# Kernel optimization log

Hardware: AMD Instinct MI355X
Metric: run time of the kernel (lower is better)

Reference implementation:

```python
import jax, jax.numpy as jnp
import numpy as np

N_NODES = 100000


def setup_inputs() -> dict:
    key = jax.random.key(0)
    k_x, k_src, k_dst, k_w = jax.random.split(key, 4)
    X = jax.random.normal(k_x, (N_NODES, 128), dtype=jnp.float32)
    src = jax.random.randint(k_src, (3200000,), 0, N_NODES, dtype=jnp.int64)
    dst = jax.random.randint(k_dst, (3200000,), 0, N_NODES, dtype=jnp.int64)
    # Linear(2*in_channels=256 -> out_channels=128); kaiming-ish scale
    W = jax.random.normal(k_w, (256, 128), dtype=jnp.float32) * (1.0 / np.sqrt(256.0))
    b = jnp.zeros((128,), dtype=jnp.float32)
    return {"X": X, "src": src, "dst": dst, "W": W, "b": b}


def reference(X, src, dst, W, b):
    # G.v2v(X, aggr='mean'): scatter-mean of neighbor features over edges
    msg = X[src]                                              # [E, d] gather
    summed = jax.ops.segment_sum(msg, dst, num_segments=N_NODES)  # [N, d]
    deg = jax.ops.segment_sum(jnp.ones_like(dst, dtype=X.dtype), dst,
                              num_segments=N_NODES)           # [N]
    X_nbr = summed / jnp.maximum(deg, 1.0)[:, None]           # mean, safe for deg=0
    # concat self + neighbor mean, linear, relu (dropout is eval-mode no-op)
    H = jnp.concatenate([X, X_nbr], axis=1)                   # [N, 2d]
    out = jax.nn.relu(H @ W + b)                              # [N, out]
    return out
```

## Files before the change

### kernel.cpp

```cpp
#include <hip/hip_runtime.h>
#include <cstddef>
#include <cstdint>


#define NODES_PER_BLOCK 16
#define PART_SHIFT 8
#define PART_SZ 256
#define MAXP 448
#define CHUNK 4096
#define CAPP 8704

typedef __attribute__((ext_vector_type(8))) short bf16x8;
typedef __attribute__((ext_vector_type(4))) float f32x4;

__device__ __forceinline__ int clampi(int v, int hi) {
    v = v < 0 ? 0 : v;
    return v >= hi ? hi - 1 : v;
}

__device__ __forceinline__ unsigned short bf16_rne(float f) {
    unsigned int u = __float_as_uint(f);
    unsigned int r = (u + 0x7FFFu + ((u >> 16) & 1u)) >> 16;
    return (unsigned short)r;
}

__device__ __forceinline__ unsigned pack2(float a, float b) {
    return (unsigned)bf16_rne(a) | ((unsigned)bf16_rne(b) << 16);
}

__device__ __forceinline__ void acc_bf16x8(float* a, uint4 r) {
    a[0] += __uint_as_float(r.x << 16);
    a[1] += __uint_as_float(r.x & 0xFFFF0000u);
    a[2] += __uint_as_float(r.y << 16);
    a[3] += __uint_as_float(r.y & 0xFFFF0000u);
    a[4] += __uint_as_float(r.z << 16);
    a[5] += __uint_as_float(r.z & 0xFFFF0000u);
    a[6] += __uint_as_float(r.w << 16);
    a[7] += __uint_as_float(r.w & 0xFFFF0000u);
}

__device__ __forceinline__ int wave_excl_scan64(int v, int lane) {
    int x = v;
#pragma unroll
    for (int off = 1; off < 64; off <<= 1) {
        int y = __shfl_up(x, off, 64);
        if (lane >= off) x += y;
    }
    return x - v;
}

__global__ void zero_cursors(int* __restrict__ c, int P) {
    int i = blockIdx.x * blockDim.x + threadIdx.x;
    if (i < P) c[i] = 0;
}

__global__ __launch_bounds__(256) void xw_to_bf16(
    const float* __restrict__ X, unsigned short* __restrict__ Xb, int total4,
    const float* __restrict__ W, unsigned short* __restrict__ Wswz)
{
    int i = blockIdx.x * blockDim.x + threadIdx.x;
    if (i < 256 * 128) {
        int k = i >> 7, n = i & 127;
        int kk = k >> 5, q = (k >> 3) & 3, j = k & 7;
        int cg = n >> 4, nn = n & 15;
        int lane = q * 16 + nn;
        Wswz[((size_t)(kk * 8 + cg) * 64 + lane) * 8 + j] =
            bf16_rne(W[(size_t)k * 128 + n]);
    }
    if (i < total4) {
        float4 v = *(const float4*)(X + (size_t)i * 4);
        ushort4 o;
        o.x = bf16_rne(v.x); o.y = bf16_rne(v.y);
        o.z = bf16_rne(v.z); o.w = bf16_rne(v.w);
        *(ushort4*)(Xb + (size_t)i * 4) = o;
    }
}

__global__ __launch_bounds__(256) void part1(
    const int* __restrict__ src, const int* __restrict__ dst,
    int* __restrict__ cursors, unsigned long long* __restrict__ parts,
    int E, int N, int P)
{
    __shared__ unsigned long long sbuf[CHUNK];
    __shared__ int hist[MAXP], base_s[MAXP], hist2[MAXP], gbase[MAXP];
    const int tid = threadIdx.x;
    const int c0  = blockIdx.x * CHUNK;
    int cnt = E - c0; if (cnt > CHUNK) cnt = CHUNK;

    for (int i = tid; i < P; i += 256) { hist[i] = 0; hist2[i] = 0; }
    __syncthreads();

    int s[16], d[16];
#pragma unroll
    for (int k = 0; k < 16; ++k) {
        int i = k * 256 + tid;
        if (i < cnt) {
            int e = c0 + i;
            d[k] = clampi(dst[e], N);
            s[k] = clampi(src[e], N);
            atomicAdd(&hist[d[k] >> PART_SHIFT], 1);
        } else {
            d[k] = -1; s[k] = 0;
        }
    }
    __syncthreads();

    if (tid < 64) {
        int pref[7]; int run = 0;
#pragma unroll
        for (int k2 = 0; k2 < 7; ++k2) {
            int idx = tid * 7 + k2;
            int v = (idx < P) ? hist[idx] : 0;
            pref[k2] = run; run += v;
        }
        int lx = wave_excl_scan64(run, tid);
#pragma unroll
        for (int k2 = 0; k2 < 7; ++k2) {
            int idx = tid * 7 + k2;
            if (idx < P) base_s[idx] = pref[k2] + lx;
        }
    }
    __syncthreads();

    for (int i = tid; i < P; i += 256) {
        int c = hist[i];
        gbase[i] = (c > 0) ? atomicAdd(&cursors[i], c) : 0;
    }
    __syncthreads();

#pragma unroll
    for (int k = 0; k < 16; ++k) {
        if (d[k] >= 0) {
            int p = d[k] >> PART_SHIFT;
            int pos = atomicAdd(&hist2[p], 1) + base_s[p];
            sbuf[pos] = ((unsigned long long)(unsigned)d[k] << 32) |
                        (unsigned)s[k];
        }
    }
    __syncthreads();

    for (int i = tid; i < cnt; i += 256) {
        unsigned long long rec = sbuf[i];
        int p = ((int)(rec >> 32)) >> PART_SHIFT;
        int gidx = gbase[p] + (i - base_s[p]);
        if (gidx < CAPP) parts[(size_t)p * CAPP + gidx] = rec;
    }
}

__global__ void scan_pbase(const int* __restrict__ cursors,
                           int* __restrict__ pbase, int P)
{
    int tid = threadIdx.x;
    int pref[7]; int run = 0;
#pragma unroll
    for (int k = 0; k < 7; ++k) {
        int idx = tid * 7 + k;
        int v = 0;
        if (idx < P) { v = cursors[idx]; if (v > CAPP) v = CAPP; }
        pref[k] = run; run += v;
    }
    int lx = wave_excl_scan64(run, tid);
#pragma unroll
    for (int k = 0; k < 7; ++k) {
        int idx = tid * 7 + k;
        if (idx < P) pbase[idx] = pref[k] + lx;
    }
}

__global__ __launch_bounds__(256) void part2(
    const unsigned long long* __restrict__ parts,
    const int* __restrict__ cursors, const int* __restrict__ pbase,
    int* __restrict__ csr, int* __restrict__ offsets, int* __restrict__ deg,
    int N, int P)
{
    __shared__ int ldeg[PART_SZ], loff[PART_SZ], lcur[PART_SZ];
    const int p   = blockIdx.x;
    const int tid = threadIdx.x;
    int cnt = cursors[p]; if (cnt > CAPP) cnt = CAPP;
    const int nbase = p << PART_SHIFT;
    const unsigned long long* prec = parts + (size_t)p * CAPP;

    ldeg[tid] = 0; lcur[tid] = 0;
    __syncthreads();
    for (int i = tid; i < cnt; i += 256) {
        int dl = ((int)(prec[i] >> 32)) & (PART_SZ - 1);
        atomicAdd(&ldeg[dl], 1);
    }
    __syncthreads();
    if (tid < 64) {
        int pref[4]; int run = 0;
#pragma unroll
        for (int k = 0; k < 4; ++k) { pref[k] = run; run += ldeg[tid * 4 + k]; }
        int lx = wave_excl_scan64(run, tid);
#pragma unroll
        for (int k = 0; k < 4; ++k) loff[tid * 4 + k] = pref[k] + lx;
    }
    __syncthreads();
    const int pb = pbase[p];
    const int n = nbase + tid;
    if (n < N) { offsets[n] = pb + loff[tid]; deg[n] = ldeg[tid]; }
    for (int i = tid; i < cnt; i += 256) {
        unsigned long long rec = prec[i];
        int dl = ((int)(rec >> 32)) & (PART_SZ - 1);
        int pos = atomicAdd(&lcur[dl], 1);
        csr[pb + loff[dl] + pos] = (int)(rec & 0xFFFFFFFFu);
    }
}

__global__ __launch_bounds__(128) void gather_gemm(
    const unsigned short* __restrict__ Xb,
    const int* __restrict__ csr,
    const int* __restrict__ offsets,
    const int* __restrict__ deg,
    const unsigned short* __restrict__ Wswz,
    const float* __restrict__ bias,
    float* __restrict__ out, int N)
{
    __shared__ unsigned short Hb[NODES_PER_BLOCK][256];
    const int tid = threadIdx.x;
    const int n0  = blockIdx.x * NODES_PER_BLOCK;

    {
        const int sub = tid & 15;
        const int grp = tid >> 4;
        const int f0  = sub * 8;
        for (int ii = 0; ii < 2; ++ii) {
            const int i = grp * 2 + ii;
            const int n = n0 + i;
            if (n >= N) continue;
            const int dg = deg[n];
            const int* brow = csr + offsets[n];
            float acc[8] = {0.f, 0.f, 0.f, 0.f, 0.f, 0.f, 0.f, 0.f};
            int t = 0;
            for (; t + 8 <= dg; t += 8) {
                int i0 = brow[t],     i1 = brow[t + 1];
                int i2 = brow[t + 2], i3 = brow[t + 3];
                int i4 = brow[t + 4], i5 = brow[t + 5];
                int i6 = brow[t + 6], i7 = brow[t + 7];
                uint4 r0 = *(const uint4*)(Xb + (size_t)i0 * 128 + f0);
                uint4 r1 = *(const uint4*)(Xb + (size_t)i1 * 128 + f0);
                uint4 r2 = *(const uint4*)(Xb + (size_t)i2 * 128 + f0);
                uint4 r3 = *(const uint4*)(Xb + (size_t)i3 * 128 + f0);
                uint4 r4 = *(const uint4*)(Xb + (size_t)i4 * 128 + f0);
                uint4 r5 = *(const uint4*)(Xb + (size_t)i5 * 128 + f0);
                uint4 r6 = *(const uint4*)(Xb + (size_t)i6 * 128 + f0);
                uint4 r7 = *(const uint4*)(Xb + (size_t)i7 * 128 + f0);
                acc_bf16x8(acc, r0); acc_bf16x8(acc, r1);
                acc_bf16x8(acc, r2); acc_bf16x8(acc, r3);
                acc_bf16x8(acc, r4); acc_bf16x8(acc, r5);
                acc_bf16x8(acc, r6); acc_bf16x8(acc, r7);
            }
            for (; t + 4 <= dg; t += 4) {
                int i0 = brow[t],     i1 = brow[t + 1];
                int i2 = brow[t + 2], i3 = brow[t + 3];
                uint4 r0 = *(const uint4*)(Xb + (size_t)i0 * 128 + f0);
                uint4 r1 = *(const uint4*)(Xb + (size_t)i1 * 128 + f0);
                uint4 r2 = *(const uint4*)(Xb + (size_t)i2 * 128 + f0);
                uint4 r3 = *(const uint4*)(Xb + (size_t)i3 * 128 + f0);
                acc_bf16x8(acc, r0); acc_bf16x8(acc, r1);
                acc_bf16x8(acc, r2); acc_bf16x8(acc, r3);
            }
            for (; t < dg; ++t) {
                uint4 r0 = *(const uint4*)(Xb + (size_t)brow[t] * 128 + f0);
                acc_bf16x8(acc, r0);
            }
            const float inv = 1.0f / fmaxf((float)dg, 1.0f);
            *(uint4*)&Hb[i][f0] = *(const uint4*)(Xb + (size_t)n * 128 + f0);
            uint4 mo;
            mo.x = pack2(acc[0] * inv, acc[1] * inv);
            mo.y = pack2(acc[2] * inv, acc[3] * inv);
            mo.z = pack2(acc[4] * inv, acc[5] * inv);
            mo.w = pack2(acc[6] * inv, acc[7] * inv);
            *(uint4*)&Hb[i][128 + f0] = mo;
        }
    }
    __syncthreads();

    const int lane = tid & 63;
    const int wv   = tid >> 6;
    const int m    = lane & 15;
    const int quad = lane >> 4;
    f32x4 acc0 = {0.f, 0.f, 0.f, 0.f};
    f32x4 acc1 = {0.f, 0.f, 0.f, 0.f};
    f32x4 acc2 = {0.f, 0.f, 0.f, 0.f};
    f32x4 acc3 = {0.f, 0.f, 0.f, 0.f};
#pragma unroll
    for (int kk = 0; kk < 8; ++kk) {
        bf16x8 a = *(const bf16x8*)&Hb[m][kk * 32 + quad * 8];
        const unsigned short* wp =
            Wswz + ((size_t)(kk * 8 + wv * 4) * 64 + lane) * 8;
        bf16x8 b0 = *(const bf16x8*)(wp);
        bf16x8 b1 = *(const bf16x8*)(wp + 64 * 8);
        bf16x8 b2 = *(const bf16x8*)(wp + 2 * 64 * 8);
        bf16x8 b3 = *(const bf16x8*)(wp + 3 * 64 * 8);
        acc0 = __builtin_amdgcn_mfma_f32_16x16x32_bf16(a, b0, acc0, 0, 0, 0);
        acc1 = __builtin_amdgcn_mfma_f32_16x16x32_bf16(a, b1, acc1, 0, 0, 0);
        acc2 = __builtin_amdgcn_mfma_f32_16x16x32_bf16(a, b2, acc2, 0, 0, 0);
        acc3 = __builtin_amdgcn_mfma_f32_16x16x32_bf16(a, b3, acc3, 0, 0, 0);
    }
    f32x4 accs[4] = {acc0, acc1, acc2, acc3};
#pragma unroll
    for (int c = 0; c < 4; ++c) {
        int feat = wv * 64 + c * 16 + m;
        float bv = bias[feat];
#pragma unroll
        for (int r = 0; r < 4; ++r) {
            int node = n0 + quad * 4 + r;
            if (node < N)
                out[(size_t)node * 128 + feat] = fmaxf(accs[c][r] + bv, 0.f);
        }
    }
}

static inline size_t align256(size_t x) { return (x + 255) & ~(size_t)255; }

extern "C" void kernel_launch(void* const* d_in, const int* in_sizes, int n_in,
                              void* d_out, int out_size, void* d_ws, size_t ws_size,
                              hipStream_t stream) {
    const float* X    = (const float*)d_in[0];
    const int*   src  = (const int*)d_in[1];
    const int*   dst  = (const int*)d_in[2];
    const float* W    = (const float*)d_in[3];
    const float* bias = (const float*)d_in[4];
    float* out = (float*)d_out;

    const int N = in_sizes[0] / 128;
    const int E = in_sizes[1];
    const int P = (N + PART_SZ - 1) >> PART_SHIFT;

    char* base = (char*)d_ws;
    size_t o_cursors = 0;
    size_t o_pbase   = o_cursors + align256((size_t)P * 4);
    size_t o_deg     = o_pbase   + align256((size_t)P * 4);
    size_t o_off     = o_deg     + align256((size_t)N * 4);
    size_t o_csr     = o_off     + align256((size_t)N * 4);
    size_t o_parts   = o_csr     + align256((size_t)E * 4);
    size_t o_wswz    = o_parts   + align256((size_t)N * 128 * 2);

    int* cursors = (int*)(base + o_cursors);
    int* pbase   = (int*)(base + o_pbase);
    int* deg     = (int*)(base + o_deg);
    int* offsets = (int*)(base + o_off);
    int* csr     = (int*)(base + o_csr);
    unsigned long long* parts = (unsigned long long*)(base + o_parts);
    unsigned short* Xb   = (unsigned short*)(base + o_parts);
    unsigned short* Wswz = (unsigned short*)(base + o_wswz);

    zero_cursors<<<(P + 255) / 256, 256, 0, stream>>>(cursors, P);

    part1<<<(E + CHUNK - 1) / CHUNK, 256, 0, stream>>>(
        src, dst, cursors, parts, E, N, P);

    scan_pbase<<<1, 64, 0, stream>>>(cursors, pbase, P);

    part2<<<P, 256, 0, stream>>>(parts, cursors, pbase, csr, offsets, deg, N, P);

    const int total4 = (N * 128) / 4;
    xw_to_bf16<<<(total4 + 255) / 256, 256, 0, stream>>>(X, Xb, total4, W, Wswz);

    gather_gemm<<<(N + NODES_PER_BLOCK - 1) / NODES_PER_BLOCK, 128, 0, stream>>>(
        Xb, csr, offsets, deg, Wswz, bias, out, N);
}
```

Before: 316.2 us.

## Fuse bf16 conversion into partition kernel, drop pbase scan and second atomic pass

Merges the X/W bf16 conversion into the first partition kernel as extra blocks when the workspace is big enough, so the conversion runs concurrently with edge binning. It also removes the global scan of partition bases by giving each partition a fixed CAPP-sized slot in the CSR array. The second shared-memory atomic pass in part1 is replaced by reusing the ranks returned by the first histogram atomics. The cost is a larger workspace, plus a fallback path that still uses the old aliasing and an extra launch.

```diff
diff --git a/kernel.cpp b/kernel.cpp
--- a/kernel.cpp
+++ b/kernel.cpp
@@ -54,11 +54,11 @@
     if (i < P) c[i] = 0;
 }
 
-__global__ __launch_bounds__(256) void xw_to_bf16(
+__device__ void do_xw_block(int xb,
     const float* __restrict__ X, unsigned short* __restrict__ Xb, int total4,
     const float* __restrict__ W, unsigned short* __restrict__ Wswz)
 {
-    int i = blockIdx.x * blockDim.x + threadIdx.x;
+    int i = xb * 256 + threadIdx.x;
     if (i < 256 * 128) {
         int k = i >> 7, n = i & 127;
         int kk = k >> 5, q = (k >> 3) & 3, j = k & 7;
@@ -76,21 +76,27 @@
     }
 }
 
-__global__ __launch_bounds__(256) void part1(
+__global__ __launch_bounds__(256) void pre1(
     const int* __restrict__ src, const int* __restrict__ dst,
     int* __restrict__ cursors, unsigned long long* __restrict__ parts,
-    int E, int N, int P)
+    int E, int N, int P, int nPart1,
+    const float* __restrict__ X, unsigned short* __restrict__ Xb, int total4,
+    const float* __restrict__ W, unsigned short* __restrict__ Wswz)
 {
+    if ((int)blockIdx.x >= nPart1) {
+        do_xw_block((int)blockIdx.x - nPart1, X, Xb, total4, W, Wswz);
+        return;
+    }
     __shared__ unsigned long long sbuf[CHUNK];
-    __shared__ int hist[MAXP], base_s[MAXP], hist2[MAXP], gbase[MAXP];
+    __shared__ int hist[MAXP], base_s[MAXP], gbase[MAXP];
     const int tid = threadIdx.x;
     const int c0  = blockIdx.x * CHUNK;
     int cnt = E - c0; if (cnt > CHUNK) cnt = CHUNK;
 
-    for (int i = tid; i < P; i += 256) { hist[i] = 0; hist2[i] = 0; }
-    __syncthreads();
-
-    int s[16], d[16];
+    for (int i = tid; i < P; i += 256) hist[i] = 0;
+    __syncthreads();
+
+    int s[16], d[16], r[16];
 #pragma unroll
     for (int k = 0; k < 16; ++k) {
         int i = k * 256 + tid;
@@ -98,9 +104,9 @@
             int e = c0 + i;
             d[k] = clampi(dst[e], N);
             s[k] = clampi(src[e], N);
-            atomicAdd(&hist[d[k] >> PART_SHIFT], 1);
+            r[k] = atomicAdd(&hist[d[k] >> PART_SHIFT], 1);
         } else {
-            d[k] = -1; s[k] = 0;
+            d[k] = -1; s[k] = 0; r[k] = 0;
         }
     }
     __syncthreads();
@@ -132,9 +138,8 @@
     for (int k = 0; k < 16; ++k) {
         if (d[k] >= 0) {
             int p = d[k] >> PART_SHIFT;
-            int pos = atomicAdd(&hist2[p], 1) + base_s[p];
-            sbuf[pos] = ((unsigned long long)(unsigned)d[k] << 32) |
-                        (unsigned)s[k];
+            sbuf[base_s[p] + r[k]] =
+                ((unsigned long long)(unsigned)d[k] << 32) | (unsigned)s[k];
         }
     }
     __syncthreads();
@@ -147,29 +152,9 @@
     }
 }
 
-__global__ void scan_pbase(const int* __restrict__ cursors,
-                           int* __restrict__ pbase, int P)
-{
-    int tid = threadIdx.x;
-    int pref[7]; int run = 0;
-#pragma unroll
-    for (int k = 0; k < 7; ++k) {
-        int idx = tid * 7 + k;
-        int v = 0;
-        if (idx < P) { v = cursors[idx]; if (v > CAPP) v = CAPP; }
-        pref[k] = run; run += v;
-    }
-    int lx = wave_excl_scan64(run, tid);
-#pragma unroll
-    for (int k = 0; k < 7; ++k) {
-        int idx = tid * 7 + k;
-        if (idx < P) pbase[idx] = pref[k] + lx;
-    }
-}
-
 __global__ __launch_bounds__(256) void part2(
     const unsigned long long* __restrict__ parts,
-    const int* __restrict__ cursors, const int* __restrict__ pbase,
+    const int* __restrict__ cursors,
     int* __restrict__ csr, int* __restrict__ offsets, int* __restrict__ deg,
     int N, int P)
 {
@@ -196,7 +181,7 @@
         for (int k = 0; k < 4; ++k) loff[tid * 4 + k] = pref[k] + lx;
     }
     __syncthreads();
-    const int pb = pbase[p];
+    const int pb = p * CAPP;
     const int n = nbase + tid;
     if (n < N) { offsets[n] = pb + loff[tid]; deg[n] = ldeg[tid]; }
     for (int i = tid; i < cnt; i += 256) {
@@ -330,33 +315,42 @@
 
     char* base = (char*)d_ws;
     size_t o_cursors = 0;
-    size_t o_pbase   = o_cursors + align256((size_t)P * 4);
-    size_t o_deg     = o_pbase   + align256((size_t)P * 4);
+    size_t o_deg     = o_cursors + align256((size_t)P * 4);
     size_t o_off     = o_deg     + align256((size_t)N * 4);
     size_t o_csr     = o_off     + align256((size_t)N * 4);
-    size_t o_parts   = o_csr     + align256((size_t)E * 4);
-    size_t o_wswz    = o_parts   + align256((size_t)N * 128 * 2);
+    size_t o_parts   = o_csr     + align256((size_t)P * CAPP * 4);
+    size_t o_wswz    = o_parts   + align256((size_t)P * CAPP * 8);
+    size_t o_xb      = o_wswz    + align256((size_t)256 * 128 * 2);
+    size_t need_big  = o_xb + (size_t)N * 128 * 2;
 
     int* cursors = (int*)(base + o_cursors);
-    int* pbase   = (int*)(base + o_pbase);
     int* deg     = (int*)(base + o_deg);
     int* offsets = (int*)(base + o_off);
     int* csr     = (int*)(base + o_csr);
     unsigned long long* parts = (unsigned long long*)(base + o_parts);
-    unsigned short* Xb   = (unsigned short*)(base + o_parts);
     unsigned short* Wswz = (unsigned short*)(base + o_wswz);
 
+    const bool big = (ws_size >= need_big);
+    unsigned short* Xb = big ? (unsigned short*)(base + o_xb)
+                             : (unsigned short*)(base + o_parts);
+
+    const int nPart1 = (E + CHUNK - 1) / CHUNK;
+    const int total4 = (N * 128) / 4;
+    const int nXw    = (total4 + 255) / 256;
+
     zero_cursors<<<(P + 255) / 256, 256, 0, stream>>>(cursors, P);
 
-    part1<<<(E + CHUNK - 1) / CHUNK, 256, 0, stream>>>(
-        src, dst, cursors, parts, E, N, P);
-
-    scan_pbase<<<1, 64, 0, stream>>>(cursors, pbase, P);
-
-    part2<<<P, 256, 0, stream>>>(parts, cursors, pbase, csr, offsets, deg, N, P);
-
-    const int total4 = (N * 128) / 4;
-    xw_to_bf16<<<(total4 + 255) / 256, 256, 0, stream>>>(X, Xb, total4, W, Wswz);
+    if (big) {
+        pre1<<<nPart1 + nXw, 256, 0, stream>>>(
+            src, dst, cursors, parts, E, N, P, nPart1, X, Xb, total4, W, Wswz);
+        part2<<<P, 256, 0, stream>>>(parts, cursors, csr, offsets, deg, N, P);
+    } else {
+        pre1<<<nPart1, 256, 0, stream>>>(
+            src, dst, cursors, parts, E, N, P, nPart1, X, Xb, total4, W, Wswz);
+        part2<<<P, 256, 0, stream>>>(parts, cursors, csr, offsets, deg, N, P);
+        pre1<<<nXw, 256, 0, stream>>>(
+            src, dst, cursors, parts, E, N, P, 0, X, Xb, total4, W, Wswz);
+    }
 
     gather_gemm<<<(N + NODES_PER_BLOCK - 1) / NODES_PER_BLOCK, 128, 0, stream>>>(
         Xb, csr, offsets, deg, Wswz, bias, out, N);
```

After: 312.7 us. No clear change (-1.1%).
